# Kernel tuning notes

Hardware: AMD Instinct MI355X
Metric: run time of the kernel (lower is better)

The kernel has to match this reference:

```python
import jax, jax.numpy as jnp
import numpy as np

K = 9          # number of umbrella neighbors (excluding self)
BN_EPS = 1e-5


def setup_inputs() -> dict:
    key = jax.random.key(0)
    ks = jax.random.split(key, 8)
    B, N, C = 4, 8192, 3
    ch = 7
    x = jax.random.normal(ks[0], (B, N, C), jnp.float32)
    w1 = jax.random.normal(ks[1], (ch, ch), jnp.float32) * 0.4
    gamma1 = jnp.ones((ch,), jnp.float32)
    beta1 = jnp.zeros((ch,), jnp.float32)
    w2 = jax.random.normal(ks[2], (ch, ch), jnp.float32) * 0.4
    bias2 = jax.random.normal(ks[3], (ch,), jnp.float32) * 0.1
    gamma2 = jnp.ones((ch,), jnp.float32)
    beta2 = jnp.zeros((ch,), jnp.float32)
    w3 = jax.random.normal(ks[4], (ch, ch), jnp.float32) * 0.4
    bias3 = jax.random.normal(ks[5], (ch,), jnp.float32) * 0.1
    return dict(x=x, w1=w1, gamma1=gamma1, beta1=beta1, w2=w2, bias2=bias2,
                gamma2=gamma2, beta2=beta2, w3=w3, bias3=bias3)


def _bn(t, gamma, beta):
    # BatchNorm2d in training mode: batch stats over (B, N, K) per channel (last dim)
    m = t.mean(axis=(0, 1, 2))
    v = t.var(axis=(0, 1, 2))  # biased, matching torch BN normalization
    return (t - m) * jax.lax.rsqrt(v + BN_EPS) * gamma + beta


def reference(x, w1, gamma1, beta1, w2, bias2, gamma2, beta2, w3, bias3):
    B, N, _ = x.shape
    # ---- kNN (negative squared distance, top-k largest == nearest) ----
    xsq = jnp.sum(x * x, axis=-1)                       # [B,N]
    xx = jnp.einsum('bnc,bmc->bnm', x, x)               # [B,N,N]
    dist = 2.0 * xx - xsq[:, :, None] - xsq[:, None, :]
    idx = jax.lax.top_k(dist, K + 1)[1]                 # [B,N,K+1], includes self
    # ---- gather neighbor coords, recenter, drop self ----
    nbr = jax.vmap(lambda xb, ib: xb[ib])(x, idx)       # [B,N,K+1,3]
    nbr = nbr - x[:, :, None, :]
    nbr = nbr[:, :, 1:, :]                              # [B,N,K,3]
    # ---- sort neighbors by azimuth phi ----
    phi = jnp.arctan2(nbr[..., 1], nbr[..., 0]) / (2.0 * np.pi) + 0.5
    order = jnp.argsort(phi, axis=-1)                   # [B,N,K]
    srt = jnp.take_along_axis(nbr, order[..., None], axis=2)  # [B,N,K,3]
    # ---- umbrella pairs: (v_i, v_{i+1 mod K}) ----
    v1 = srt
    v2 = jnp.roll(srt, -1, axis=2)
    centroids = 0.5 * (v1 + v2)                         # [B,N,K,3]
    normals = jnp.cross(v1, v2) + 1e-5
    normals = normals / jnp.linalg.norm(normals, axis=-1, keepdims=True)
    # flip so the first normal's x-component is positive (per point)
    pos_mask = (normals[:, :, 0:1, 0] > 0).astype(x.dtype) * 2.0 - 1.0  # [B,N,1]
    normals = normals * pos_mask[..., None]
    positions = jnp.sum(centroids * normals, axis=-1) / jnp.sqrt(jnp.asarray(3.0, x.dtype))
    feat = jnp.concatenate([centroids, normals, positions[..., None]], axis=-1)  # [B,N,K,7]
    # ---- tiny 1x1 conv MLP (channel-last einsum) + BN + ReLU ----
    h = jnp.einsum('bnkc,oc->bnko', feat, w1)
    h = jax.nn.relu(_bn(h, gamma1, beta1))
    h = jnp.einsum('bnkc,oc->bnko', h, w2) + bias2
    h = jax.nn.relu(_bn(h, gamma2, beta2))
    h = jnp.einsum('bnkc,oc->bnko', h, w3) + bias3
    pooled = jnp.max(h, axis=2)                         # [B,N,7]
    return jnp.concatenate([x, pooled], axis=-1)        # [B,N,10]
```

## Files before the change

### kernel.cpp

```cpp
#include <hip/hip_runtime.h>
#include <math.h>

#define BB 4
#define NN 8192
#define TOTAL (BB*NN)
#define KNBR 9
#define CH 7
#define NCHUNK 16
#define CHUNK (NN/NCHUNK)
#define SLOTS 8
#define NROWS (NCHUNK*SLOTS/2)
#define QB 4
#define BN_EPS 1e-5f
#define M_ELEMS (TOTAL*KNBR)
#define NREP 16
#define NBLK 256

#define OFF_PTS   0
#define OFF_PI    524288
#define OFF_STATS 8912896
#define OFF_H1    8914944

__device__ __forceinline__ void ibody(float (&dl)[10], int (&il)[10], float d, int ii) {
    bool c0 = d > dl[0];
#pragma unroll
    for (int p = 9; p > 0; p--) {
        bool here = d > dl[p];
        bool up   = d > dl[p-1];
        float nd = up ? dl[p-1] : d;
        int   ni = up ? il[p-1] : ii;
        if (here) { dl[p] = nd; il[p] = ni; }
    }
    if (c0) { dl[0] = d; il[0] = ii; }
}

__device__ __forceinline__ void insert10(float (&dl)[10], int (&il)[10], float d, int ii) {
    if (d > dl[9]) ibody(dl, il, d, ii);
}

__global__ __launch_bounds__(256) void knn_k(const float* __restrict__ x,
                                             float4* __restrict__ pts,
                                             unsigned int* __restrict__ pi,
                                             float* __restrict__ stats) {
    const int b = blockIdx.z, chunk = blockIdx.y;
    const int c0 = chunk * CHUNK;

    if (blockIdx.x == 0 && blockIdx.y == 0 && blockIdx.z == 0) {
        for (int i = threadIdx.x; i < NREP*28 + 8; i += 256) stats[i] = 0.f;
    }

    __shared__ float4 tile[CHUNK];
    if (threadIdx.x < CHUNK/4) {
        const float4* __restrict__ x4 = (const float4*)(x + (long)(b*NN + c0)*3);
        int t = threadIdx.x;
        float4 f0 = x4[3*t], f1 = x4[3*t+1], f2 = x4[3*t+2];
        float px[4] = {f0.x, f0.w, f1.z, f2.y};
        float py[4] = {f0.y, f1.x, f1.w, f2.z};
        float pz[4] = {f0.z, f1.y, f2.x, f2.w};
#pragma unroll
        for (int u = 0; u < 4; u++) {
            float sq = __fadd_rn(__fadd_rn(__fmul_rn(px[u],px[u]), __fmul_rn(py[u],py[u])),
                                 __fmul_rn(pz[u],pz[u]));
            tile[4*t+u] = make_float4(px[u], py[u], pz[u], sq);
        }
    }
    __syncthreads();

    if (blockIdx.x == 0) {
#pragma unroll
        for (int j = 0; j < CHUNK/256; j++)
            pts[b*NN + c0 + threadIdx.x + j*256] = tile[threadIdx.x + j*256];
    }

    const int q0 = blockIdx.x * (256*QB) + threadIdx.x;
    float qx2[QB], qy2[QB], qz2[QB], nqb[QB];
#pragma unroll
    for (int v = 0; v < QB; v++) {
        long qoff = (long)(b*NN + q0 + v*256) * 3;
        float qx = x[qoff], qy = x[qoff+1], qz = x[qoff+2];
        float qw = qx*qx + qy*qy + qz*qz;
        qx2[v] = qx + qx; qy2[v] = qy + qy; qz2[v] = qz + qz;
        nqb[v] = -1.0f - qw;
    }

    unsigned int m[QB][SLOTS];
#pragma unroll
    for (int v = 0; v < QB; v++)
#pragma unroll
        for (int s = 0; s < SLOTS; s++) m[v][s] = 0xFFFFFFFFu;

#pragma unroll 4
    for (int j = 0; j < CHUNK; j++) {
        float4 t = tile[j];
#pragma unroll
        for (int v = 0; v < QB; v++) {
            float d = fmaf(qx2[v], t.x, fmaf(qy2[v], t.y, fmaf(qz2[v], t.z, nqb[v] - t.w)));
            unsigned int kd = (__float_as_uint(d) & 0xFFFFFE00u) | (unsigned int)j;
#pragma unroll
            for (int p = SLOTS-1; p >= 1; p--)
                asm("v_med3_u32 %0, %1, %2, %3" : "=v"(m[v][p]) : "v"(kd), "v"(m[v][p-1]), "v"(m[v][p]));
            m[v][0] = kd < m[v][0] ? kd : m[v][0];
        }
    }

#pragma unroll
    for (int v = 0; v < QB; v++) {
        int idx[SLOTS];
#pragma unroll
        for (int s = 0; s < SLOTS; s++) idx[s] = (int)(m[v][s] & 511u);
#pragma unroll
        for (int r = 0; r < SLOTS; r++) {
#pragma unroll
            for (int i = (r & 1); i + 1 < SLOTS; i += 2) {
                int a = idx[i], c = idx[i+1];
                idx[i] = min(a, c); idx[i+1] = max(a, c);
            }
        }
        int g = b*NN + q0 + v*256;
#pragma unroll
        for (int s2 = 0; s2 < SLOTS/2; s2++) {
            unsigned int lo = (unsigned int)(c0 + idx[2*s2]);
            unsigned int hi = (unsigned int)(c0 + idx[2*s2+1]);
            pi[(long)(chunk*(SLOTS/2) + s2)*TOTAL + g] = lo | (hi << 16);
        }
    }
}

__global__ __launch_bounds__(128) void geom_k(const float4* __restrict__ pts,
                                              const unsigned int* __restrict__ pi,
                                              const float* __restrict__ w1,
                                              float* __restrict__ h1, float* __restrict__ stats) {
    __shared__ float sw1[49];
    __shared__ float acc[14];
    if (threadIdx.x < 49) sw1[threadIdx.x] = w1[threadIdx.x];
    if (threadIdx.x < 14) acc[threadIdx.x] = 0.f;
    __syncthreads();

    int g = blockIdx.x * 128 + threadIdx.x;
    int b = g >> 13, n = g & (NN-1);
    const float4* __restrict__ base = pts + b*NN;
    float4 qp = base[n];
    float qn = -qp.w;

    float dl[10]; int il[10];
#pragma unroll
    for (int j = 0; j < 10; j++) { dl[j] = -INFINITY; il[j] = 0; }
#pragma unroll
    for (int h = 0; h < 2; h++) {
        unsigned int pk[32];
#pragma unroll
        for (int u = 0; u < 32; u++) pk[u] = pi[(long)(h*32 + u)*TOTAL + g];
#pragma unroll
        for (int bt = 0; bt < 4; bt++) {
            int id[16];
#pragma unroll
            for (int u = 0; u < 8; u++) {
                id[2*u]   = (int)(pk[bt*8 + u] & 0xFFFFu);
                id[2*u+1] = (int)(pk[bt*8 + u] >> 16);
            }
            float4 pp[16];
#pragma unroll
            for (int v = 0; v < 16; v++) pp[v] = base[id[v]];
            float dd[16];
#pragma unroll
            for (int v = 0; v < 16; v++) {
                float dot2 = __fadd_rn(__fadd_rn(__fmul_rn(qp.x, 2.f*pp[v].x),
                                                 __fmul_rn(qp.y, 2.f*pp[v].y)),
                                       __fmul_rn(qp.z, 2.f*pp[v].z));
                dd[v] = __fsub_rn(__fadd_rn(dot2, qn), pp[v].w);
            }
#pragma unroll
            for (int v = 0; v < 16; v++) insert10(dl, il, dd[v], id[v]);
        }
    }

    float vx[9], vy[9], vz[9], ph[9];
#pragma unroll
    for (int t = 0; t < 9; t++) {
        float4 p4 = base[il[t+1]];
        vx[t] = p4.x - qp.x; vy[t] = p4.y - qp.y; vz[t] = p4.z - qp.z;
        ph[t] = atan2f(vy[t], vx[t]) / 6.283185307179586f + 0.5f;
    }

    int rank[9];
#pragma unroll
    for (int t = 0; t < 9; t++) {
        int r = 0;
#pragma unroll
        for (int u = 0; u < 9; u++) {
            if (u == t) continue;
            bool before = (ph[u] < ph[t]) || (ph[u] == ph[t] && u < t);
            r += before ? 1 : 0;
        }
        rank[t] = r;
    }
    float sx[9], sy[9], sz[9];
#pragma unroll
    for (int s = 0; s < 9; s++) {
        float a = 0.f, bb = 0.f, c = 0.f;
#pragma unroll
        for (int t = 0; t < 9; t++) {
            bool m = (rank[t] == s);
            a = m ? vx[t] : a; bb = m ? vy[t] : bb; c = m ? vz[t] : c;
        }
        sx[s] = a; sy[s] = bb; sz[s] = c;
    }

    float sgn;
    {
        float ax = sx[0], ay = sy[0], az = sz[0];
        float bx = sx[1], by = sy[1], bz = sz[1];
        float nx0 = ay*bz - az*by + 1e-5f;
        float ny0 = az*bx - ax*bz + 1e-5f;
        float nz0 = ax*by - ay*bx + 1e-5f;
        float inv = 1.0f / sqrtf(nx0*nx0 + ny0*ny0 + nz0*nz0);
        sgn = (nx0*inv > 0.0f) ? 1.0f : -1.0f;
    }

    float sum[7], sumsq[7];
#pragma unroll
    for (int o = 0; o < 7; o++) { sum[o] = 0.f; sumsq[o] = 0.f; }

#pragma unroll
    for (int t = 0; t < 9; t++) {
        const int t2 = (t + 1) % 9;
        float ax = sx[t],  ay = sy[t],  az = sz[t];
        float bx = sx[t2], by = sy[t2], bz = sz[t2];
        float cx = 0.5f*(ax+bx), cy = 0.5f*(ay+by), cz = 0.5f*(az+bz);
        float nx0 = ay*bz - az*by + 1e-5f;
        float ny0 = az*bx - ax*bz + 1e-5f;
        float nz0 = ax*by - ay*bx + 1e-5f;
        float inv = 1.0f / sqrtf(nx0*nx0 + ny0*ny0 + nz0*nz0);
        float nx = nx0*inv*sgn, ny = ny0*inv*sgn, nz = nz0*inv*sgn;
        float pos = (cx*nx + cy*ny + cz*nz) / 1.7320508075688772f;

        float f[7] = {cx, cy, cz, nx, ny, nz, pos};
        float* outp = h1 + ((long)g*9 + t) * 7;
#pragma unroll
        for (int o = 0; o < 7; o++) {
            float h = 0.f;
#pragma unroll
            for (int c = 0; c < 7; c++) h += f[c] * sw1[o*7 + c];
            outp[o] = h;
            sum[o] += h; sumsq[o] += h*h;
        }
    }

#pragma unroll
    for (int o = 0; o < 7; o++) {
        float s  = sum[o];
        float s2 = sumsq[o];
        for (int off = 32; off > 0; off >>= 1) { s += __shfl_down(s, off); s2 += __shfl_down(s2, off); }
        if ((threadIdx.x & 63) == 0) {
            atomicAdd(&acc[o], s);
            atomicAdd(&acc[7 + o], s2);
        }
    }
    __syncthreads();
    if (threadIdx.x < 14)
        atomicAdd(&stats[(blockIdx.x & (NREP-1))*28 + threadIdx.x], acc[threadIdx.x]);
}

__device__ __forceinline__ void grid_barrier(int* cnt) {
    __syncthreads();
    if (threadIdx.x == 0) {
        __threadfence();
        __hip_atomic_fetch_add(cnt, 1, __ATOMIC_RELEASE, __HIP_MEMORY_SCOPE_AGENT);
        while (__hip_atomic_load(cnt, __ATOMIC_ACQUIRE, __HIP_MEMORY_SCOPE_AGENT) < NBLK)
            __builtin_amdgcn_s_sleep(8);
    }
    __syncthreads();
}

__global__ __launch_bounds__(128) void tail_k(const float* __restrict__ x,
                                              const float* __restrict__ h1,
                                              const float* __restrict__ gamma1, const float* __restrict__ beta1,
                                              const float* __restrict__ w2, const float* __restrict__ bias2,
                                              const float* __restrict__ gamma2, const float* __restrict__ beta2,
                                              const float* __restrict__ w3, const float* __restrict__ bias3,
                                              float* __restrict__ stats, float* __restrict__ out) {
    __shared__ float sw2[49], sw3[49], sb2[7], sb3[7];
    __shared__ float acc[14];
    __shared__ float sco[14];
    if (threadIdx.x < 49) { sw2[threadIdx.x] = w2[threadIdx.x]; sw3[threadIdx.x] = w3[threadIdx.x]; }
    if (threadIdx.x < 7)  { sb2[threadIdx.x] = bias2[threadIdx.x]; sb3[threadIdx.x] = bias3[threadIdx.x]; }
    if (threadIdx.x < 14) acc[threadIdx.x] = 0.f;
    __syncthreads();

    int* cnt = (int*)(stats + NREP*28);
    int g = blockIdx.x * 128 + threadIdx.x;
    const float invM = 1.0f / (float)M_ELEMS;

    float s1v[7], b1v[7];
#pragma unroll
    for (int c = 0; c < 7; c++) {
        float sm = 0.f, sq = 0.f;
#pragma unroll
        for (int r = 0; r < NREP; r++) { sm += stats[r*28 + c]; sq += stats[r*28 + 7 + c]; }
        float m = sm * invM;
        float v = sq * invM - m*m;
        float sc = gamma1[c] / sqrtf(v + BN_EPS);
        s1v[c] = sc; b1v[c] = beta1[c] - m*sc;
    }

    float hv[63];
    float sum[7], sumsq[7];
#pragma unroll
    for (int o = 0; o < 7; o++) { sum[o] = 0.f; sumsq[o] = 0.f; }
    const float* hh = h1 + (long)g * 63;
#pragma unroll
    for (int t = 0; t < 9; t++) {
        float a[7];
#pragma unroll
        for (int c = 0; c < 7; c++) a[c] = fmaxf(hh[t*7 + c]*s1v[c] + b1v[c], 0.0f);
#pragma unroll
        for (int o = 0; o < 7; o++) {
            float h = 0.f;
#pragma unroll
            for (int c = 0; c < 7; c++) h += a[c] * sw2[o*7 + c];
            h += sb2[o];
            hv[t*7 + o] = h;
            sum[o] += h; sumsq[o] += h*h;
        }
    }
#pragma unroll
    for (int o = 0; o < 7; o++) {
        float s  = sum[o];
        float s2 = sumsq[o];
        for (int off = 32; off > 0; off >>= 1) { s += __shfl_down(s, off); s2 += __shfl_down(s2, off); }
        if ((threadIdx.x & 63) == 0) {
            atomicAdd(&acc[o], s);
            atomicAdd(&acc[7 + o], s2);
        }
    }
    __syncthreads();
    if (threadIdx.x < 14)
        atomicAdd(&stats[(blockIdx.x & (NREP-1))*28 + 14 + threadIdx.x], acc[threadIdx.x]);

    grid_barrier(cnt);

    if (threadIdx.x < 7) {
        int c = threadIdx.x;
        float sm = 0.f, sq = 0.f;
#pragma unroll
        for (int r = 0; r < NREP; r++) {
            sm += __hip_atomic_load(&stats[r*28 + 14 + c], __ATOMIC_RELAXED, __HIP_MEMORY_SCOPE_AGENT);
            sq += __hip_atomic_load(&stats[r*28 + 21 + c], __ATOMIC_RELAXED, __HIP_MEMORY_SCOPE_AGENT);
        }
        float m = sm * invM;
        float v = sq * invM - m*m;
        float sc = gamma2[c] / sqrtf(v + BN_EPS);
        sco[c] = sc; sco[7 + c] = beta2[c] - m*sc;
    }
    __syncthreads();

    float pooled[7];
#pragma unroll
    for (int o = 0; o < 7; o++) pooled[o] = -INFINITY;
#pragma unroll
    for (int t = 0; t < 9; t++) {
        float a[7];
#pragma unroll
        for (int c = 0; c < 7; c++) a[c] = fmaxf(hv[t*7 + c]*sco[c] + sco[7 + c], 0.0f);
#pragma unroll
        for (int o = 0; o < 7; o++) {
            float h = 0.f;
#pragma unroll
            for (int c = 0; c < 7; c++) h += a[c] * sw3[o*7 + c];
            h += sb3[o];
            pooled[o] = fmaxf(pooled[o], h);
        }
    }
    out[g*10 + 0] = x[g*3 + 0];
    out[g*10 + 1] = x[g*3 + 1];
    out[g*10 + 2] = x[g*3 + 2];
#pragma unroll
    for (int o = 0; o < 7; o++) out[g*10 + 3 + o] = pooled[o];
}

extern "C" void kernel_launch(void* const* d_in, const int* in_sizes, int n_in,
                              void* d_out, int out_size, void* d_ws, size_t ws_size,
                              hipStream_t stream) {
    const float* x      = (const float*)d_in[0];
    const float* w1     = (const float*)d_in[1];
    const float* gamma1 = (const float*)d_in[2];
    const float* beta1  = (const float*)d_in[3];
    const float* w2     = (const float*)d_in[4];
    const float* bias2  = (const float*)d_in[5];
    const float* gamma2 = (const float*)d_in[6];
    const float* beta2  = (const float*)d_in[7];
    const float* w3     = (const float*)d_in[8];
    const float* bias3  = (const float*)d_in[9];
    float* out = (float*)d_out;

    char* ws = (char*)d_ws;
    float4*       pts  = (float4*)(ws + OFF_PTS);
    unsigned int* pi   = (unsigned int*)(ws + OFF_PI);
    float*        stats= (float*)(ws + OFF_STATS);
    float*        h1   = (float*)(ws + OFF_H1);

    knn_k <<<dim3(NN/(256*QB), NCHUNK, BB), 256, 0, stream>>>(x, pts, pi, stats);
    geom_k<<<TOTAL/128, 128, 0, stream>>>(pts, pi, w1, h1, stats);
    tail_k<<<NBLK, 128, 0, stream>>>(x, h1, gamma1, beta1, w2, bias2,
                                     gamma2, beta2, w3, bias3, stats, out);
}
```

Baseline: 231.8 us.

## Keep approximate keys per candidate and preselect 16 before exact distance recheck

The chunked kNN pass now stores each of its 8 candidates per chunk as a 32-bit key: the truncated approximate distance bits in the high part and the global index in the low 13 bits. The geometry kernel then runs a med3 selection over all 128 keys to pick the best 16, and gathers and recomputes exact distances only for those, instead of 128 candidates. This removes most of the random point gathers and exact insertions, at the cost of twice the candidate buffer traffic and the risk that the truncated keys drop a true top-10 neighbor.

```diff
diff --git a/kernel.cpp b/kernel.cpp
--- a/kernel.cpp
+++ b/kernel.cpp
@@ -9,7 +9,8 @@
 #define NCHUNK 16
 #define CHUNK (NN/NCHUNK)
 #define SLOTS 8
-#define NROWS (NCHUNK*SLOTS/2)
+#define NROWS (NCHUNK*SLOTS)
+#define GSEL 16
 #define QB 4
 #define BN_EPS 1e-5f
 #define M_ELEMS (TOTAL*KNBR)
@@ -18,8 +19,8 @@
 
 #define OFF_PTS   0
 #define OFF_PI    524288
-#define OFF_STATS 8912896
-#define OFF_H1    8914944
+#define OFF_STATS 17301504
+#define OFF_H1    17303552
 
 __device__ __forceinline__ void ibody(float (&dl)[10], int (&il)[10], float d, int ii) {
     bool c0 = d > dl[0];
@@ -105,23 +106,12 @@
 
 #pragma unroll
     for (int v = 0; v < QB; v++) {
-        int idx[SLOTS];
-#pragma unroll
-        for (int s = 0; s < SLOTS; s++) idx[s] = (int)(m[v][s] & 511u);
-#pragma unroll
-        for (int r = 0; r < SLOTS; r++) {
-#pragma unroll
-            for (int i = (r & 1); i + 1 < SLOTS; i += 2) {
-                int a = idx[i], c = idx[i+1];
-                idx[i] = min(a, c); idx[i+1] = max(a, c);
-            }
-        }
         int g = b*NN + q0 + v*256;
 #pragma unroll
-        for (int s2 = 0; s2 < SLOTS/2; s2++) {
-            unsigned int lo = (unsigned int)(c0 + idx[2*s2]);
-            unsigned int hi = (unsigned int)(c0 + idx[2*s2+1]);
-            pi[(long)(chunk*(SLOTS/2) + s2)*TOTAL + g] = lo | (hi << 16);
+        for (int s = 0; s < SLOTS; s++) {
+            unsigned int mm = m[v][s];
+            unsigned int key = (mm & 0xFFFFE000u) | (unsigned int)(c0 + (int)(mm & 511u));
+            pi[(long)(chunk*SLOTS + s)*TOTAL + g] = key;
         }
     }
 }
@@ -142,36 +132,53 @@
     float4 qp = base[n];
     float qn = -qp.w;
 
+    unsigned int mk[GSEL];
+#pragma unroll
+    for (int s = 0; s < GSEL; s++) mk[s] = 0xFFFFFFFFu;
+#pragma unroll
+    for (int h = 0; h < 4; h++) {
+        unsigned int pk[32];
+#pragma unroll
+        for (int u = 0; u < 32; u++) pk[u] = pi[(long)(h*32 + u)*TOTAL + g];
+#pragma unroll
+        for (int u = 0; u < 32; u++) {
+            unsigned int kd = pk[u];
+#pragma unroll
+            for (int p = GSEL-1; p >= 1; p--)
+                asm("v_med3_u32 %0, %1, %2, %3" : "=v"(mk[p]) : "v"(kd), "v"(mk[p-1]), "v"(mk[p]));
+            mk[0] = kd < mk[0] ? kd : mk[0];
+        }
+    }
+
+    int idx[GSEL];
+#pragma unroll
+    for (int s = 0; s < GSEL; s++) idx[s] = (int)(mk[s] & 8191u);
+#pragma unroll
+    for (int r = 0; r < GSEL; r++) {
+#pragma unroll
+        for (int i = (r & 1); i + 1 < GSEL; i += 2) {
+            int a = idx[i], c = idx[i+1];
+            idx[i] = min(a, c); idx[i+1] = max(a, c);
+        }
+    }
+
     float dl[10]; int il[10];
 #pragma unroll
     for (int j = 0; j < 10; j++) { dl[j] = -INFINITY; il[j] = 0; }
-#pragma unroll
-    for (int h = 0; h < 2; h++) {
-        unsigned int pk[32];
-#pragma unroll
-        for (int u = 0; u < 32; u++) pk[u] = pi[(long)(h*32 + u)*TOTAL + g];
-#pragma unroll
-        for (int bt = 0; bt < 4; bt++) {
-            int id[16];
-#pragma unroll
-            for (int u = 0; u < 8; u++) {
-                id[2*u]   = (int)(pk[bt*8 + u] & 0xFFFFu);
-                id[2*u+1] = (int)(pk[bt*8 + u] >> 16);
-            }
-            float4 pp[16];
-#pragma unroll
-            for (int v = 0; v < 16; v++) pp[v] = base[id[v]];
-            float dd[16];
-#pragma unroll
-            for (int v = 0; v < 16; v++) {
-                float dot2 = __fadd_rn(__fadd_rn(__fmul_rn(qp.x, 2.f*pp[v].x),
-                                                 __fmul_rn(qp.y, 2.f*pp[v].y)),
-                                       __fmul_rn(qp.z, 2.f*pp[v].z));
-                dd[v] = __fsub_rn(__fadd_rn(dot2, qn), pp[v].w);
-            }
-#pragma unroll
-            for (int v = 0; v < 16; v++) insert10(dl, il, dd[v], id[v]);
-        }
+    {
+        float4 pp[GSEL];
+#pragma unroll
+        for (int v = 0; v < GSEL; v++) pp[v] = base[idx[v]];
+        float dd[GSEL];
+#pragma unroll
+        for (int v = 0; v < GSEL; v++) {
+            float dot2 = __fadd_rn(__fadd_rn(__fmul_rn(qp.x, 2.f*pp[v].x),
+                                             __fmul_rn(qp.y, 2.f*pp[v].y)),
+                                   __fmul_rn(qp.z, 2.f*pp[v].z));
+            dd[v] = __fsub_rn(__fadd_rn(dot2, qn), pp[v].w);
+        }
+#pragma unroll
+        for (int v = 0; v < GSEL; v++) insert10(dl, il, dd[v], idx[v]);
     }
 
     float vx[9], vy[9], vz[9], ph[9];
```

After: 220.4 us. 4.9% less time.
